# Kernel optimization log

Measured on AMD Instinct MI355X. Metric: run time of the kernel, lower is better.

## Reference

```python
import jax, jax.numpy as jnp
import numpy as np


def setup_inputs() -> dict:
    key = jax.random.key(0)
    k1, k2 = jax.random.split(key)
    B, D, N = 8, 3, 8192
    preds = jax.random.normal(k1, (B, D, N), dtype=jnp.float32)
    gts = jax.random.normal(k2, (B, D, N), dtype=jnp.float32)
    return {"preds": preds, "gts": gts}


def _chamfer(preds, gts):
    # preds, gts: [B, 3, N] -> x, y: [B, N, 3]
    x = jnp.swapaxes(preds, 2, 1)
    y = jnp.swapaxes(gts, 2, 1)
    # Squared-norm rows/cols + cross term: P[b,i,j] = |x_i|^2 + |y_j|^2 - 2 x_i.y_j
    rx = jnp.sum(x * x, axis=-1)              # [B, Nx]
    ry = jnp.sum(y * y, axis=-1)              # [B, Ny]
    zz = jnp.einsum("bnd,bmd->bnm", x, y)     # [B, Nx, Ny]
    P = rx[:, :, None] + ry[:, None, :] - 2.0 * zz
    loss_1 = jnp.sum(jnp.min(P, axis=1))      # nearest pred for each gt
    loss_2 = jnp.sum(jnp.min(P, axis=2))      # nearest gt for each pred
    return loss_1 + loss_2


def reference(preds, gts):
    return _chamfer(preds, gts)
```

## Files before the change

### kernel.cpp

```cpp
#include <hip/hip_runtime.h>
#include <hip/hip_bf16.h>


#define CN 8192
#define BQ 2048
#define IPT 8
#define SPLITS 8
#define RB (CN / SPLITS)
#define TILE 512
#define NBATCH 8
#define QCHUNKS (CN / BQ)

__global__ __launch_bounds__(256) void chamfer_partial(
    const float* __restrict__ preds, const float* __restrict__ gts,
    float* __restrict__ partial) {
  const int bid = blockIdx.x;
  const int s     = bid & (SPLITS - 1);
  const int qc    = (bid >> 3) & (QCHUNKS - 1);
  const int batch = (bid >> 5) & (NBATCH - 1);
  const int dir   = bid >> 8;

  const float* __restrict__ Qb = (dir ? gts : preds) + batch * 3 * CN;
  const float* __restrict__ Rb = (dir ? preds : gts) + batch * 3 * CN;

  const int tid = threadIdx.x;

  float x0[IPT], x1[IPT], x2[IPT], mm[IPT];
#pragma unroll
  for (int k = 0; k < IPT; ++k) {
    const int q = qc * BQ + k * 256 + tid;
    x0[k] = Qb[q];
    x1[k] = Qb[CN + q];
    x2[k] = Qb[2 * CN + q];
    mm[k] = -INFINITY;
  }

  __shared__ float4 ytile[TILE];
  const int rbase = s * RB;

  for (int t0i = 0; t0i < RB; t0i += TILE) {
    __syncthreads();
#pragma unroll
    for (int k = 0; k < TILE / 256; ++k) {
      const int r = rbase + t0i + k * 256 + tid;
      const float y0 = Rb[r];
      const float y1 = Rb[CN + r];
      const float y2 = Rb[2 * CN + r];
      ytile[k * 256 + tid] = make_float4(
          y0, y1, y2, -0.5f * fmaf(y0, y0, fmaf(y1, y1, y2 * y2)));
    }
    __syncthreads();

#pragma unroll 2
    for (int j = 0; j < TILE; j += 2) {
      const float4 ya = ytile[j];
      const float4 yb = ytile[j + 1];
#pragma unroll
      for (int k = 0; k < IPT; ++k) {
        const float ta =
            fmaf(x2[k], ya.z, fmaf(x1[k], ya.y, fmaf(x0[k], ya.x, ya.w)));
        const float tb =
            fmaf(x2[k], yb.z, fmaf(x1[k], yb.y, fmaf(x0[k], yb.x, yb.w)));
        mm[k] = fmaxf(fmaxf(mm[k], ta), tb);
      }
    }
  }

  float* __restrict__ P =
      partial +
      (size_t)(((dir * NBATCH + batch) * QCHUNKS + qc) * SPLITS + s) * BQ;
#pragma unroll
  for (int k = 0; k < IPT; ++k) {
    const float rx = fmaf(x0[k], x0[k], fmaf(x1[k], x1[k], x2[k] * x2[k]));
    P[k * 256 + tid] = fmaf(mm[k], -2.0f, rx);
  }
}

__global__ __launch_bounds__(256) void chamfer_reduce(
    const float* __restrict__ partial, double* __restrict__ acc) {
  const int tid = threadIdx.x;
  const int g = blockIdx.x * 256 + tid;
  const int qlocal = g & (BQ - 1);
  const int grp = g >> 11;

  const float* __restrict__ P = partial + (size_t)grp * (SPLITS * BQ) + qlocal;
  float m = P[0];
#pragma unroll
  for (int s2 = 1; s2 < SPLITS; ++s2) m = fminf(m, P[s2 * BQ]);

  float v = m;
#pragma unroll
  for (int off = 32; off > 0; off >>= 1) v += __shfl_down(v, off, 64);

  __shared__ float wsum[4];
  if ((tid & 63) == 0) wsum[tid >> 6] = v;
  __syncthreads();
  if (tid == 0) {
    const float b = wsum[0] + wsum[1] + wsum[2] + wsum[3];
    atomicAdd(acc, (double)b);
  }
}

__global__ void chamfer_finalize(const double* __restrict__ acc,
                                 float* __restrict__ out) {
  out[0] = (float)acc[0];
}

extern "C" void kernel_launch(void* const* d_in, const int* in_sizes, int n_in,
                              void* d_out, int out_size, void* d_ws, size_t ws_size,
                              hipStream_t stream) {
  const float* preds = (const float*)d_in[0];
  const float* gts   = (const float*)d_in[1];

  double* acc      = (double*)d_ws;
  float*  partial  = (float*)((char*)d_ws + 256);

  hipMemsetAsync(d_ws, 0, 8, stream);
  chamfer_partial<<<512, 256, 0, stream>>>(preds, gts, partial);
  chamfer_reduce<<<512, 256, 0, stream>>>(partial, acc);
  chamfer_finalize<<<1, 1, 0, stream>>>(acc, (float*)d_out);
}
```

Measured before the change: 144.3 us.

## Prepack points as float4, read reference points directly from global, fuse finalize

```diff
diff --git a/kernel.cpp b/kernel.cpp
--- a/kernel.cpp
+++ b/kernel.cpp
@@ -3,16 +3,32 @@
 
 
 #define CN 8192
+#define NBATCH 8
 #define BQ 2048
 #define IPT 8
 #define SPLITS 8
 #define RB (CN / SPLITS)
-#define TILE 512
-#define NBATCH 8
 #define QCHUNKS (CN / BQ)
 
+__global__ __launch_bounds__(256) void chamfer_pack(
+    const float* __restrict__ preds, const float* __restrict__ gts,
+    float4* __restrict__ ppack, float4* __restrict__ gpack,
+    double* __restrict__ acc, unsigned* __restrict__ cnt) {
+  const int g = blockIdx.x * 256 + threadIdx.x;
+  if (g == 0) { *acc = 0.0; *cnt = 0u; }
+  const int batch = g >> 13, i = g & (CN - 1);
+  const float* __restrict__ P = preds + batch * 3 * CN;
+  const float p0 = P[i], p1 = P[CN + i], p2 = P[2 * CN + i];
+  ppack[g] =
+      make_float4(p0, p1, p2, -0.5f * fmaf(p0, p0, fmaf(p1, p1, p2 * p2)));
+  const float* __restrict__ G = gts + batch * 3 * CN;
+  const float g0 = G[i], g1 = G[CN + i], g2 = G[2 * CN + i];
+  gpack[g] =
+      make_float4(g0, g1, g2, -0.5f * fmaf(g0, g0, fmaf(g1, g1, g2 * g2)));
+}
+
 __global__ __launch_bounds__(256) void chamfer_partial(
-    const float* __restrict__ preds, const float* __restrict__ gts,
+    const float4* __restrict__ ppack, const float4* __restrict__ gpack,
     float* __restrict__ partial) {
   const int bid = blockIdx.x;
   const int s     = bid & (SPLITS - 1);
@@ -20,49 +36,35 @@
   const int batch = (bid >> 5) & (NBATCH - 1);
   const int dir   = bid >> 8;
 
-  const float* __restrict__ Qb = (dir ? gts : preds) + batch * 3 * CN;
-  const float* __restrict__ Rb = (dir ? preds : gts) + batch * 3 * CN;
-
+  const float4* __restrict__ Qp = (dir ? gpack : ppack) + batch * CN;
+  const float4* __restrict__ Rp = (dir ? ppack : gpack) + batch * CN + s * RB;
   const int tid = threadIdx.x;
 
-  float x0[IPT], x1[IPT], x2[IPT], mm[IPT];
+  float x0[IPT], x1[IPT], x2[IPT], xw[IPT], mm[IPT];
 #pragma unroll
   for (int k = 0; k < IPT; ++k) {
-    const int q = qc * BQ + k * 256 + tid;
-    x0[k] = Qb[q];
-    x1[k] = Qb[CN + q];
-    x2[k] = Qb[2 * CN + q];
+    const float4 v = Qp[qc * BQ + k * 256 + tid];
+    x0[k] = v.x; x1[k] = v.y; x2[k] = v.z; xw[k] = v.w;
     mm[k] = -INFINITY;
   }
 
-  __shared__ float4 ytile[TILE];
-  const int rbase = s * RB;
-
-  for (int t0i = 0; t0i < RB; t0i += TILE) {
-    __syncthreads();
+  for (int j = 0; j < RB; j += 4) {
+    const float4 ya = Rp[j];
+    const float4 yb = Rp[j + 1];
+    const float4 yc = Rp[j + 2];
+    const float4 yd = Rp[j + 3];
 #pragma unroll
-    for (int k = 0; k < TILE / 256; ++k) {
-      const int r = rbase + t0i + k * 256 + tid;
-      const float y0 = Rb[r];
-      const float y1 = Rb[CN + r];
-      const float y2 = Rb[2 * CN + r];
-      ytile[k * 256 + tid] = make_float4(
-          y0, y1, y2, -0.5f * fmaf(y0, y0, fmaf(y1, y1, y2 * y2)));
-    }
-    __syncthreads();
-
-#pragma unroll 2
-    for (int j = 0; j < TILE; j += 2) {
-      const float4 ya = ytile[j];
-      const float4 yb = ytile[j + 1];
-#pragma unroll
-      for (int k = 0; k < IPT; ++k) {
-        const float ta =
-            fmaf(x2[k], ya.z, fmaf(x1[k], ya.y, fmaf(x0[k], ya.x, ya.w)));
-        const float tb =
-            fmaf(x2[k], yb.z, fmaf(x1[k], yb.y, fmaf(x0[k], yb.x, yb.w)));
-        mm[k] = fmaxf(fmaxf(mm[k], ta), tb);
-      }
+    for (int k = 0; k < IPT; ++k) {
+      const float ta =
+          fmaf(x2[k], ya.z, fmaf(x1[k], ya.y, fmaf(x0[k], ya.x, ya.w)));
+      const float tb =
+          fmaf(x2[k], yb.z, fmaf(x1[k], yb.y, fmaf(x0[k], yb.x, yb.w)));
+      const float tc =
+          fmaf(x2[k], yc.z, fmaf(x1[k], yc.y, fmaf(x0[k], yc.x, yc.w)));
+      const float td =
+          fmaf(x2[k], yd.z, fmaf(x1[k], yd.y, fmaf(x0[k], yd.x, yd.w)));
+      asm("v_max3_f32 %0, %0, %1, %2" : "+v"(mm[k]) : "v"(ta), "v"(tb));
+      asm("v_max3_f32 %0, %0, %1, %2" : "+v"(mm[k]) : "v"(tc), "v"(td));
     }
   }
 
@@ -70,14 +72,12 @@
       partial +
       (size_t)(((dir * NBATCH + batch) * QCHUNKS + qc) * SPLITS + s) * BQ;
 #pragma unroll
-  for (int k = 0; k < IPT; ++k) {
-    const float rx = fmaf(x0[k], x0[k], fmaf(x1[k], x1[k], x2[k] * x2[k]));
-    P[k * 256 + tid] = fmaf(mm[k], -2.0f, rx);
-  }
+  for (int k = 0; k < IPT; ++k) P[k * 256 + tid] = -2.0f * (xw[k] + mm[k]);
 }
 
 __global__ __launch_bounds__(256) void chamfer_reduce(
-    const float* __restrict__ partial, double* __restrict__ acc) {
+    const float* __restrict__ partial, double* __restrict__ acc,
+    unsigned* __restrict__ cnt, float* __restrict__ out) {
   const int tid = threadIdx.x;
   const int g = blockIdx.x * 256 + tid;
   const int qlocal = g & (BQ - 1);
@@ -96,14 +96,14 @@
   if ((tid & 63) == 0) wsum[tid >> 6] = v;
   __syncthreads();
   if (tid == 0) {
-    const float b = wsum[0] + wsum[1] + wsum[2] + wsum[3];
-    atomicAdd(acc, (double)b);
+    atomicAdd(acc, (double)(wsum[0] + wsum[1] + wsum[2] + wsum[3]));
+    __threadfence();
+    const unsigned t = atomicAdd(cnt, 1u);
+    if (t == gridDim.x - 1) {
+      const double total = atomicAdd(acc, 0.0);
+      out[0] = (float)total;
+    }
   }
-}
-
-__global__ void chamfer_finalize(const double* __restrict__ acc,
-                                 float* __restrict__ out) {
-  out[0] = (float)acc[0];
 }
 
 extern "C" void kernel_launch(void* const* d_in, const int* in_sizes, int n_in,
@@ -112,11 +112,13 @@
   const float* preds = (const float*)d_in[0];
   const float* gts   = (const float*)d_in[1];
 
-  double* acc      = (double*)d_ws;
-  float*  partial  = (float*)((char*)d_ws + 256);
+  double*   acc     = (double*)d_ws;
+  unsigned* cnt     = (unsigned*)((char*)d_ws + 8);
+  float4*   ppack   = (float4*)((char*)d_ws + 256);
+  float4*   gpack   = (float4*)((char*)d_ws + 256 + (size_t)NBATCH * CN * 16);
+  float*    partial = (float*)((char*)d_ws + 256 + (size_t)2 * NBATCH * CN * 16);
 
-  hipMemsetAsync(d_ws, 0, 8, stream);
-  chamfer_partial<<<512, 256, 0, stream>>>(preds, gts, partial);
-  chamfer_reduce<<<512, 256, 0, stream>>>(partial, acc);
-  chamfer_finalize<<<1, 1, 0, stream>>>(acc, (float*)d_out);
+  chamfer_pack<<<256, 256, 0, stream>>>(preds, gts, ppack, gpack, acc, cnt);
+  chamfer_partial<<<512, 256, 0, stream>>>(ppack, gpack, partial);
+  chamfer_reduce<<<512, 256, 0, stream>>>(partial, acc, cnt, (float*)d_out);
 }
```

Result: slower. 202.0 us (+40.0%).
